# Optimization experiments

Measured on AMD Instinct MI355X. Metric: run time of the kernel, lower is better.

The kernel has to match this reference:

```python
import jax, jax.numpy as jnp
import numpy as np
from jax import lax

B, CIN, COUT, H, W = 4, 256, 256, 64, 64
KH = KW = 3
K = KH * KW
GN_GROUPS = 32
EPS = 1e-5


def setup_inputs() -> dict:
    key = jax.random.key(0)
    ks = jax.random.split(key, 6)
    x = jax.random.normal(ks[0], (B, CIN, H, W), jnp.float32)
    # offset predictor conv: 3x3, 18 out channels, with bias (init small so offsets stay near 0)
    offset_w = jax.random.normal(ks[1], (2 * K, CIN, KH, KW), jnp.float32) * 0.01
    offset_b = jax.random.normal(ks[2], (2 * K,), jnp.float32) * 0.01
    # deformable conv weight (no bias), He-ish scale
    deform_w = jax.random.normal(ks[3], (COUT, CIN, KH, KW), jnp.float32) * (1.0 / np.sqrt(CIN * K))
    gn_gamma = jnp.ones((COUT,), jnp.float32)
    gn_beta = jnp.zeros((COUT,), jnp.float32)
    return {"x": x, "offset_w": offset_w, "offset_b": offset_b,
            "deform_w": deform_w, "gn_gamma": gn_gamma, "gn_beta": gn_beta}


def _deform_conv(x, offset, weight):
    """Deformable conv v1, stride=1, pad=1, dil=1, deformable_groups=1.
    x: [B,C,H,W]; offset: [B,2K,H,W] with (dy,dx) per kernel tap; weight: [O,C,3,3].
    """
    b, c, h, w = x.shape
    off = offset.reshape(b, K, 2, h, w)
    # base sampling grid per kernel tap: p = p0 - pad + k
    ky, kx = jnp.meshgrid(jnp.arange(KH), jnp.arange(KW), indexing="ij")
    base_y = (jnp.arange(h, dtype=jnp.float32) - 1.0)[None, :, None] + ky.reshape(K).astype(jnp.float32)[:, None, None]  # [K,H,1]
    base_x = (jnp.arange(w, dtype=jnp.float32) - 1.0)[None, None, :] + kx.reshape(K).astype(jnp.float32)[:, None, None]  # [K,1,W]
    py = base_y[None] + off[:, :, 0]  # [B,K,H,W]
    px = base_x[None] + off[:, :, 1]  # [B,K,H,W]

    y0 = jnp.floor(py)
    x0 = jnp.floor(px)
    ty = py - y0
    tx = px - x0
    y0 = y0.astype(jnp.int32)
    x0 = x0.astype(jnp.int32)

    x_hw = x.transpose(0, 2, 3, 1).reshape(b, h * w, c)  # [B,HW,C]

    def corner(yi, xi, wgt):
        valid = (yi >= 0) & (yi < h) & (xi >= 0) & (xi < w)
        yc = jnp.clip(yi, 0, h - 1)
        xc = jnp.clip(xi, 0, w - 1)
        idx = (yc * w + xc).reshape(b, K * h * w)
        v = jnp.take_along_axis(x_hw, idx[..., None], axis=1)  # [B,KHW,C]
        return v * (wgt * valid.astype(wgt.dtype)).reshape(b, K * h * w, 1)

    samp = (corner(y0, x0, (1 - ty) * (1 - tx))
            + corner(y0, x0 + 1, (1 - ty) * tx)
            + corner(y0 + 1, x0, ty * (1 - tx))
            + corner(y0 + 1, x0 + 1, ty * tx))  # [B,KHW,C]
    samp = samp.reshape(b, K, h, w, c)
    return jnp.einsum("bkhwc,ock->bohw", samp, weight.reshape(weight.shape[0], c, K))


def reference(x, offset_w, offset_b, deform_w, gn_gamma, gn_beta):
    # offset = conv3x3(x) + bias
    offset = lax.conv_general_dilated(
        x, offset_w, window_strides=(1, 1), padding=((1, 1), (1, 1)),
        dimension_numbers=("NCHW", "OIHW", "NCHW")) + offset_b[None, :, None, None]
    out = _deform_conv(x, offset, deform_w)
    # GroupNorm(32, COUT) + ReLU
    b, c, h, w = out.shape
    g = out.reshape(b, GN_GROUPS, (c // GN_GROUPS) * h * w)
    mu = g.mean(axis=2, keepdims=True)
    var = g.var(axis=2, keepdims=True)
    g = (g - mu) * lax.rsqrt(var + EPS)
    out = g.reshape(b, c, h, w) * gn_gamma[None, :, None, None] + gn_beta[None, :, None, None]
    return jax.nn.relu(out)
```

## Files before the change

kernel.cpp:

```cpp
#include <hip/hip_runtime.h>
#include <hip/hip_bf16.h>
#include <stdint.h>


typedef unsigned short u16;
typedef __bf16 bf16x8 __attribute__((ext_vector_type(8)));
typedef float f32x4_t __attribute__((ext_vector_type(4)));

#define HW 4096

__device__ __forceinline__ uint32_t f32_to_bf16_rne(float f) {
  uint32_t u = __builtin_bit_cast(uint32_t, f);
  return (u + 0x7FFFu + ((u >> 16) & 1u)) >> 16;
}
__device__ __forceinline__ float bf_lo(uint32_t u) {
  return __builtin_bit_cast(float, u << 16);
}
__device__ __forceinline__ float bf_hi(uint32_t u) {
  return __builtin_bit_cast(float, u & 0xFFFF0000u);
}
__device__ __forceinline__ uint32_t blend2(uint32_t a, uint32_t b, uint32_t c,
                                           uint32_t d, float4 mw) {
  float lo = mw.x * bf_lo(a) + mw.y * bf_lo(b) + mw.z * bf_lo(c) + mw.w * bf_lo(d);
  float hi = mw.x * bf_hi(a) + mw.y * bf_hi(b) + mw.z * bf_hi(c) + mw.w * bf_hi(d);
  return f32_to_bf16_rne(lo) | (f32_to_bf16_rne(hi) << 16);
}

__global__ __launch_bounds__(256) void k_transpose(const float* __restrict__ x,
                                                   u16* __restrict__ xt) {
  __shared__ float tile[32][33];
  int b = blockIdx.z;
  int c0 = blockIdx.y * 32;
  int p0 = blockIdx.x * 32;
  int tx = threadIdx.x, ty = threadIdx.y;
#pragma unroll
  for (int j = 0; j < 32; j += 8)
    tile[ty + j][tx] = x[(b * 256 + c0 + ty + j) * HW + p0 + tx];
  __syncthreads();
  int wid = ty * 32 + tx;
  int cp = wid & 15;
  int pr = wid >> 4;
#pragma unroll
  for (int j = 0; j < 2; j++) {
    int p = pr + j * 16;
    uint32_t lo = f32_to_bf16_rne(tile[cp * 2][p]);
    uint32_t hi = f32_to_bf16_rne(tile[cp * 2 + 1][p]);
    *(uint32_t*)&xt[(b * HW + p0 + p) * 256 + c0 + cp * 2] = lo | (hi << 16);
  }
}

__global__ __launch_bounds__(256) void k_prep(const float* __restrict__ wsrc,
                                              const float* __restrict__ ow,
                                              u16* __restrict__ warr,
                                              u16* __restrict__ owm,
                                              float* __restrict__ part) {
  int bid = blockIdx.x;
  if (bid < 2304) {
    int e = bid * 256 + threadIdx.x;
    int kk = e & 7, m = (e >> 3) & 255, g = (e >> 11) & 7, kc = e >> 14;
    int cin = (kc & 3) * 64 + g * 8 + kk;
    int tap = kc >> 2;
    warr[e] = (u16)f32_to_bf16_rne(wsrc[m * 2304 + cin * 9 + tap]);
  } else if (bid < 2592) {
    int e = (bid - 2304) * 256 + threadIdx.x;
    int kk = e & 7, m = (e >> 3) & 31, g = (e >> 8) & 7, kc = e >> 11;
    int cin = (kc & 3) * 64 + g * 8 + kk;
    int tap = kc >> 2;
    float v = (m < 18) ? ow[m * 2304 + cin * 9 + tap] : 0.f;
    owm[e] = (u16)f32_to_bf16_rne(v);
  } else {
    part[threadIdx.x] = 0.f;
  }
}

__global__ __launch_bounds__(512, 4) void k_conv(
    const u16* __restrict__ xt, const u16* __restrict__ warr,
    const u16* __restrict__ owm, const float* __restrict__ ob,
    float* __restrict__ out, float* __restrict__ part) {
  __shared__ char smem[54272];
  u16* stage = (u16*)smem;
  float* off_part = (float*)(smem + 33792);
  int4* ci_s = (int4*)smem;
  float4* mw_s = (float4*)(smem + 4608);
  u16* b_s = (u16*)(smem + 9216);

  int tid = threadIdx.x;
  int lane = tid & 63;
  int wm = tid >> 6;
  int b = blockIdx.x >> 7;
  int pt = blockIdx.x & 127;
  int p0 = pt * 32;
  int yrow = p0 >> 6, xbase = p0 & 63;

  {
    u16* st = stage + wm * 2112;
    int q = lane & 15, pq = lane >> 4;
    int oct = lane & 7, pxs = lane >> 3;
    f32x4_t a2[2][2] = {};
#pragma unroll 1
    for (int kc = wm; kc < 36; kc += 8) {
      int tap = kc >> 2, cc = kc & 3;
      int ky = tap / 3, kx = tap % 3;
      int yy = yrow + ky - 1;
      bool vy = (yy >= 0) && (yy < 64);
#pragma unroll
      for (int i = 0; i < 4; i++) {
        int px = i * 8 + pxs;
        int xx2 = xbase + px + kx - 1;
        uint4 v = make_uint4(0u, 0u, 0u, 0u);
        if (vy && xx2 >= 0 && xx2 < 64)
          v = *(const uint4*)&xt[(b * HW + yy * 64 + xx2) * 256 + cc * 64 + oct * 8];
        *(uint4*)&st[oct * 264 + px * 8] = v;
      }
#pragma unroll
      for (int ks = 0; ks < 2; ks++) {
        int g = ks * 4 + pq;
        const u16* ab = owm + kc * 2048 + g * 256;
#pragma unroll
        for (int s = 0; s < 2; s++) {
          bf16x8 bfr = *(bf16x8*)&st[g * 264 + (s * 16 + q) * 8];
#pragma unroll
          for (int im = 0; im < 2; im++) {
            bf16x8 af = *(const bf16x8*)&ab[(im * 16 + q) * 8];
            a2[s][im] = __builtin_amdgcn_mfma_f32_16x16x32_bf16(af, bfr, a2[s][im], 0, 0, 0);
          }
        }
      }
    }
#pragma unroll
    for (int s = 0; s < 2; s++)
#pragma unroll
      for (int im = 0; im < 2; im++)
#pragma unroll
        for (int r = 0; r < 4; r++) {
          int oc = im * 16 + pq * 4 + r;
          if (oc < 18) off_part[(wm * 32 + s * 16 + q) * 20 + oc] = a2[s][im][r];
        }
  }
  __syncthreads();
  for (int it = tid; it < 288; it += 512) {
    int tap = it >> 5;
    int px = it & 31;
    float dy = ob[2 * tap], dx = ob[2 * tap + 1];
#pragma unroll
    for (int wv = 0; wv < 8; wv++) {
      dy += off_part[(wv * 32 + px) * 20 + 2 * tap];
      dx += off_part[(wv * 32 + px) * 20 + 2 * tap + 1];
    }
    int ky = tap / 3, kx = tap % 3;
    int p = p0 + px;
    int yq = p >> 6, xq = p & 63;
    float py = (float)(yq - 1 + ky) + dy;
    float pxx = (float)(xq - 1 + kx) + dx;
    float y0f = floorf(py), x0f = floorf(pxx);
    float ty = py - y0f, tx = pxx - x0f;
    int y0 = (int)y0f, x0 = (int)x0f;
    int y1 = y0 + 1, x1 = x0 + 1;
    float wy0 = 1.f - ty, wy1 = ty, wx0 = 1.f - tx, wx1 = tx;
    bool vy0 = (y0 >= 0) && (y0 < 64), vy1 = (y1 >= 0) && (y1 < 64);
    bool vx0 = (x0 >= 0) && (x0 < 64), vx1 = (x1 >= 0) && (x1 < 64);
    int cy0 = min(max(y0, 0), 63), cy1 = min(max(y1, 0), 63);
    int cx0 = min(max(x0, 0), 63), cx1 = min(max(x1, 0), 63);
    int base = b * HW;
    int4 ci;
    ci.x = (base + cy0 * 64 + cx0) * 256;
    ci.y = (base + cy0 * 64 + cx1) * 256;
    ci.z = (base + cy1 * 64 + cx0) * 256;
    ci.w = (base + cy1 * 64 + cx1) * 256;
    float4 mw;
    mw.x = wy0 * wx0 * ((vy0 && vx0) ? 1.f : 0.f);
    mw.y = wy0 * wx1 * ((vy0 && vx1) ? 1.f : 0.f);
    mw.z = wy1 * wx0 * ((vy1 && vx0) ? 1.f : 0.f);
    mw.w = wy1 * wx1 * ((vy1 && vx1) ? 1.f : 0.f);
    ci_s[it] = ci;
    mw_s[it] = mw;
  }
  __syncthreads();

  {
    int oct8 = tid & 15;
    int pxg = tid >> 4;
    int sub = pxg >> 4;
    int pxw = pxg & 15;
    int col = lane & 15;
    int pq = lane >> 4;
    f32x4_t acc[2][2] = {};

    int4 ci = ci_s[pxg];
    float4 mw = mw_s[pxg];
    int e = oct8 * 8;
    uint4 c0 = *(const uint4*)&xt[ci.x + e];
    uint4 c1 = *(const uint4*)&xt[ci.y + e];
    uint4 c2 = *(const uint4*)&xt[ci.z + e];
    uint4 c3 = *(const uint4*)&xt[ci.w + e];

#pragma unroll 1
    for (int dccg = 0; dccg < 18; dccg++) {
      u16* bb = b_s + (dccg & 1) * 4352;
      uint4 u;
      u.x = blend2(c0.x, c1.x, c2.x, c3.x, mw);
      u.y = blend2(c0.y, c1.y, c2.y, c3.y, mw);
      u.z = blend2(c0.z, c1.z, c2.z, c3.z, mw);
      u.w = blend2(c0.w, c1.w, c2.w, c3.w, mw);
      *(uint4*)&bb[sub * 2176 + oct8 * 136 + pxw * 8] = u;
      __syncthreads();
      if (dccg < 17) {
        int nx = dccg + 1;
        int tapn = nx >> 1;
        int en = (nx & 1) * 128 + oct8 * 8;
        int4 cin = ci_s[tapn * 32 + pxg];
        float4 mwn = mw_s[tapn * 32 + pxg];
        c0 = *(const uint4*)&xt[cin.x + en];
        c1 = *(const uint4*)&xt[cin.y + en];
        c2 = *(const uint4*)&xt[cin.z + en];
        c3 = *(const uint4*)&xt[cin.w + en];
        mw = mwn;
      }
      int tap = dccg >> 1, dcc = dccg & 1;
#pragma unroll
      for (int ks = 0; ks < 4; ks++) {
        int ro = ks * 4 + pq;
        bf16x8 b0 = *(bf16x8*)&bb[ro * 136 + col * 8];
        bf16x8 b1 = *(bf16x8*)&bb[2176 + ro * 136 + col * 8];
        int kc = tap * 4 + dcc * 2 + (ks >> 1);
        int g = (ks & 1) * 4 + pq;
        const u16* ab = warr + kc * 16384 + g * 2048 + (wm * 32 + col) * 8;
#pragma unroll
        for (int im = 0; im < 2; im++) {
          bf16x8 af = *(const bf16x8*)&ab[im * 128];
          acc[0][im] = __builtin_amdgcn_mfma_f32_16x16x32_bf16(af, b0, acc[0][im], 0, 0, 0);
          acc[1][im] = __builtin_amdgcn_mfma_f32_16x16x32_bf16(af, b1, acc[1][im], 0, 0, 0);
        }
      }
    }

#pragma unroll
    for (int im = 0; im < 2; im++) {
      float s = 0.f, ss = 0.f;
#pragma unroll
      for (int sb = 0; sb < 2; sb++) {
        int n = p0 + sb * 16 + col;
#pragma unroll
        for (int r = 0; r < 4; r++) {
          int m = wm * 32 + im * 16 + pq * 4 + r;
          float v = acc[sb][im][r];
          out[(b * 256 + m) * HW + n] = v;
          s += v;
          ss += v * v;
        }
      }
#pragma unroll
      for (int msk = 1; msk <= 16; msk <<= 1) {
        s += __shfl_xor(s, msk);
        ss += __shfl_xor(ss, msk);
      }
      if ((lane & 31) == 0) {
        int g = wm * 4 + im * 2 + (lane >> 5);
        float* pp = part + (b * 32 + g) * 2;
        atomicAdd(pp, s);
        atomicAdd(pp + 1, ss);
      }
    }
  }
}

__global__ __launch_bounds__(256) void k_gn_apply(float* __restrict__ out,
                                                  const float2* __restrict__ part,
                                                  const float* __restrict__ gamma,
                                                  const float* __restrict__ beta) {
  __shared__ float sga, sbe;
  int gid = blockIdx.x * 256 + threadIdx.x;
  int c = (gid >> 10) & 255;
  int bb = gid >> 18;
  if (threadIdx.x == 0) {
    float2 p = part[bb * 32 + (c >> 3)];
    float mu = p.x / 32768.f;
    float var = p.y / 32768.f - mu * mu;
    float rs = rsqrtf(var + 1e-5f);
    float ga = gamma[c] * rs;
    sga = ga;
    sbe = beta[c] - mu * ga;
  }
  __syncthreads();
  float ga = sga, be = sbe;
  float4 v = ((const float4*)out)[gid];
  v.x = fmaxf(v.x * ga + be, 0.f);
  v.y = fmaxf(v.y * ga + be, 0.f);
  v.z = fmaxf(v.z * ga + be, 0.f);
  v.w = fmaxf(v.w * ga + be, 0.f);
  ((float4*)out)[gid] = v;
}

extern "C" void kernel_launch(void* const* d_in, const int* in_sizes, int n_in,
                              void* d_out, int out_size, void* d_ws, size_t ws_size,
                              hipStream_t stream) {
  const float* x = (const float*)d_in[0];
  const float* offset_w = (const float*)d_in[1];
  const float* offset_b = (const float*)d_in[2];
  const float* deform_w = (const float*)d_in[3];
  const float* gn_gamma = (const float*)d_in[4];
  const float* gn_beta = (const float*)d_in[5];
  float* out = (float*)d_out;
  char* ws = (char*)d_ws;

  u16* xt = (u16*)ws;
  u16* warr = (u16*)(ws + 8388608);
  u16* owm = (u16*)(ws + 9568256);
  float* part = (float*)(ws + 9715712);

  k_transpose<<<dim3(128, 8, 4), dim3(32, 8), 0, stream>>>(x, xt);
  k_prep<<<dim3(2593), dim3(256), 0, stream>>>(deform_w, offset_w, warr, owm, part);
  k_conv<<<dim3(512), dim3(512), 0, stream>>>(xt, warr, owm, offset_b, out, part);
  k_gn_apply<<<dim3(4096), dim3(256), 0, stream>>>(out, (const float2*)part, gn_gamma, gn_beta);
}
```

Measured before the change: 163.4 us.

## Merge prep kernels, swizzle conv blocks, prefetch both halves, set MFMA priority

The transpose and weight-prep kernels are merged into one launch, removing a kernel boundary. The conv block index is remapped so neighbouring blocks land on different XCDs, and the gather loop is restructured per tap to prefetch both channel halves ahead of the GEMM. s_setprio is raised around the MFMA sections. GroupNorm apply now computes scale and shift per thread instead of going through shared memory and a barrier. These are several unrelated tweaks, and the extra prefetch registers may lower occupancy.

```diff
diff --git a/kernel.cpp b/kernel.cpp
--- a/kernel.cpp
+++ b/kernel.cpp
@@ -26,50 +26,48 @@
   return f32_to_bf16_rne(lo) | (f32_to_bf16_rne(hi) << 16);
 }
 
-__global__ __launch_bounds__(256) void k_transpose(const float* __restrict__ x,
-                                                   u16* __restrict__ xt) {
+__global__ __launch_bounds__(256) void k_pre(const float* __restrict__ x,
+                                             const float* __restrict__ wsrc,
+                                             const float* __restrict__ ow,
+                                             u16* __restrict__ xt,
+                                             u16* __restrict__ warr,
+                                             u16* __restrict__ owm,
+                                             float* __restrict__ part) {
   __shared__ float tile[32][33];
-  int b = blockIdx.z;
-  int c0 = blockIdx.y * 32;
-  int p0 = blockIdx.x * 32;
-  int tx = threadIdx.x, ty = threadIdx.y;
-#pragma unroll
-  for (int j = 0; j < 32; j += 8)
-    tile[ty + j][tx] = x[(b * 256 + c0 + ty + j) * HW + p0 + tx];
-  __syncthreads();
-  int wid = ty * 32 + tx;
-  int cp = wid & 15;
-  int pr = wid >> 4;
-#pragma unroll
-  for (int j = 0; j < 2; j++) {
-    int p = pr + j * 16;
-    uint32_t lo = f32_to_bf16_rne(tile[cp * 2][p]);
-    uint32_t hi = f32_to_bf16_rne(tile[cp * 2 + 1][p]);
-    *(uint32_t*)&xt[(b * HW + p0 + p) * 256 + c0 + cp * 2] = lo | (hi << 16);
-  }
-}
-
-__global__ __launch_bounds__(256) void k_prep(const float* __restrict__ wsrc,
-                                              const float* __restrict__ ow,
-                                              u16* __restrict__ warr,
-                                              u16* __restrict__ owm,
-                                              float* __restrict__ part) {
   int bid = blockIdx.x;
-  if (bid < 2304) {
-    int e = bid * 256 + threadIdx.x;
+  int tid = threadIdx.x;
+  if (bid < 4096) {
+    int bx = bid & 127, by = (bid >> 7) & 7, bz = bid >> 10;
+    int c0 = by * 32, p0 = bx * 32;
+    int tx = tid & 31, ty = tid >> 5;
+#pragma unroll
+    for (int j = 0; j < 32; j += 8)
+      tile[ty + j][tx] = x[(bz * 256 + c0 + ty + j) * HW + p0 + tx];
+    __syncthreads();
+    int cp = tid & 15;
+    int pr = tid >> 4;
+#pragma unroll
+    for (int j = 0; j < 2; j++) {
+      int p = pr + j * 16;
+      uint32_t lo = f32_to_bf16_rne(tile[cp * 2][p]);
+      uint32_t hi = f32_to_bf16_rne(tile[cp * 2 + 1][p]);
+      *(uint32_t*)&xt[(bz * HW + p0 + p) * 256 + c0 + cp * 2] = lo | (hi << 16);
+    }
+  } else if (bid < 6400) {
+    int e = (bid - 4096) * 256 + tid;
     int kk = e & 7, m = (e >> 3) & 255, g = (e >> 11) & 7, kc = e >> 14;
     int cin = (kc & 3) * 64 + g * 8 + kk;
     int tap = kc >> 2;
     warr[e] = (u16)f32_to_bf16_rne(wsrc[m * 2304 + cin * 9 + tap]);
-  } else if (bid < 2592) {
-    int e = (bid - 2304) * 256 + threadIdx.x;
+  } else if (bid < 6688) {
+    int e = (bid - 6400) * 256 + tid;
     int kk = e & 7, m = (e >> 3) & 31, g = (e >> 8) & 7, kc = e >> 11;
     int cin = (kc & 3) * 64 + g * 8 + kk;
     int tap = kc >> 2;
     float v = (m < 18) ? ow[m * 2304 + cin * 9 + tap] : 0.f;
     owm[e] = (u16)f32_to_bf16_rne(v);
   } else {
-    part[threadIdx.x] = 0.f;
+    part[tid] = 0.f;
   }
 }
 
@@ -87,8 +85,9 @@
   int tid = threadIdx.x;
   int lane = tid & 63;
   int wm = tid >> 6;
-  int b = blockIdx.x >> 7;
-  int pt = blockIdx.x & 127;
+  int wk = (blockIdx.x & 7) * 64 + (blockIdx.x >> 3);
+  int b = wk >> 7;
+  int pt = wk & 127;
   int p0 = pt * 32;
   int yrow = p0 >> 6, xbase = p0 & 63;
 
@@ -184,54 +183,73 @@
     int pxw = pxg & 15;
     int col = lane & 15;
     int pq = lane >> 4;
+    int e0 = oct8 * 8;
     f32x4_t acc[2][2] = {};
 
-    int4 ci = ci_s[pxg];
-    float4 mw = mw_s[pxg];
-    int e = oct8 * 8;
-    uint4 c0 = *(const uint4*)&xt[ci.x + e];
-    uint4 c1 = *(const uint4*)&xt[ci.y + e];
-    uint4 c2 = *(const uint4*)&xt[ci.z + e];
-    uint4 c3 = *(const uint4*)&xt[ci.w + e];
-
-#pragma unroll 1
-    for (int dccg = 0; dccg < 18; dccg++) {
-      u16* bb = b_s + (dccg & 1) * 4352;
+    auto stage_b = [&](uint4 c0, uint4 c1, uint4 c2, uint4 c3, float4 mw, u16* bb) {
       uint4 u;
       u.x = blend2(c0.x, c1.x, c2.x, c3.x, mw);
       u.y = blend2(c0.y, c1.y, c2.y, c3.y, mw);
       u.z = blend2(c0.z, c1.z, c2.z, c3.z, mw);
       u.w = blend2(c0.w, c1.w, c2.w, c3.w, mw);
       *(uint4*)&bb[sub * 2176 + oct8 * 136 + pxw * 8] = u;
-      __syncthreads();
-      if (dccg < 17) {
-        int nx = dccg + 1;
-        int tapn = nx >> 1;
-        int en = (nx & 1) * 128 + oct8 * 8;
-        int4 cin = ci_s[tapn * 32 + pxg];
-        float4 mwn = mw_s[tapn * 32 + pxg];
-        c0 = *(const uint4*)&xt[cin.x + en];
-        c1 = *(const uint4*)&xt[cin.y + en];
-        c2 = *(const uint4*)&xt[cin.z + en];
-        c3 = *(const uint4*)&xt[cin.w + en];
-        mw = mwn;
-      }
-      int tap = dccg >> 1, dcc = dccg & 1;
+    };
+    auto gemm = [&](const u16* bb, int kcbase) {
+      __builtin_amdgcn_s_setprio(1);
 #pragma unroll
       for (int ks = 0; ks < 4; ks++) {
         int ro = ks * 4 + pq;
-        bf16x8 b0 = *(bf16x8*)&bb[ro * 136 + col * 8];
-        bf16x8 b1 = *(bf16x8*)&bb[2176 + ro * 136 + col * 8];
-        int kc = tap * 4 + dcc * 2 + (ks >> 1);
-        int g = (ks & 1) * 4 + pq;
-        const u16* ab = warr + kc * 16384 + g * 2048 + (wm * 32 + col) * 8;
+        bf16x8 bb0 = *(bf16x8*)&bb[ro * 136 + col * 8];
+        bf16x8 bb1 = *(bf16x8*)&bb[2176 + ro * 136 + col * 8];
+        int kc = kcbase + (ks >> 1);
+        int gg = (ks & 1) * 4 + pq;
+        const u16* ab = warr + kc * 16384 + gg * 2048 + (wm * 32 + col) * 8;
 #pragma unroll
         for (int im = 0; im < 2; im++) {
           bf16x8 af = *(const bf16x8*)&ab[im * 128];
-          acc[0][im] = __builtin_amdgcn_mfma_f32_16x16x32_bf16(af, b0, acc[0][im], 0, 0, 0);
-          acc[1][im] = __builtin_amdgcn_mfma_f32_16x16x32_bf16(af, b1, acc[1][im], 0, 0, 0);
+          acc[0][im] = __builtin_amdgcn_mfma_f32_16x16x32_bf16(af, bb0, acc[0][im], 0, 0, 0);
+          acc[1][im] = __builtin_amdgcn_mfma_f32_16x16x32_bf16(af, bb1, acc[1][im], 0, 0, 0);
         }
       }
+      __builtin_amdgcn_s_setprio(0);
+    };
+
+    int4 ci0 = ci_s[pxg];
+    float4 mw_cur = mw_s[pxg];
+    uint4 a0 = *(const uint4*)&xt[ci0.x + e0];
+    uint4 a1 = *(const uint4*)&xt[ci0.y + e0];
+    uint4 a2v = *(const uint4*)&xt[ci0.z + e0];
+    uint4 a3 = *(const uint4*)&xt[ci0.w + e0];
+    uint4 g0 = *(const uint4*)&xt[ci0.x + 128 + e0];
+    uint4 g1 = *(const uint4*)&xt[ci0.y + 128 + e0];
+    uint4 g2 = *(const uint4*)&xt[ci0.z + 128 + e0];
+    uint4 g3 = *(const uint4*)&xt[ci0.w + 128 + e0];
+    float4 mw_nxt = mw_cur;
+    int4 ci_n = ci0;
+
+#pragma unroll 1
+    for (int dp = 0; dp < 9; dp++) {
+      stage_b(a0, a1, a2v, a3, mw_cur, b_s);
+      __syncthreads();
+      if (dp < 8) {
+        ci_n = ci_s[(dp + 1) * 32 + pxg];
+        mw_nxt = mw_s[(dp + 1) * 32 + pxg];
+        a0 = *(const uint4*)&xt[ci_n.x + e0];
+        a1 = *(const uint4*)&xt[ci_n.y + e0];
+        a2v = *(const uint4*)&xt[ci_n.z + e0];
+        a3 = *(const uint4*)&xt[ci_n.w + e0];
+      }
+      gemm(b_s, dp * 4);
+      stage_b(g0, g1, g2, g3, mw_cur, b_s + 4352);
+      __syncthreads();
+      if (dp < 8) {
+        g0 = *(const uint4*)&xt[ci_n.x + 128 + e0];
+        g1 = *(const uint4*)&xt[ci_n.y + 128 + e0];
+        g2 = *(const uint4*)&xt[ci_n.z + 128 + e0];
+        g3 = *(const uint4*)&xt[ci_n.w + 128 + e0];
+      }
+      gemm(b_s + 4352, dp * 4 + 2);
+      mw_cur = mw_nxt;
     }
 
 #pragma unroll
@@ -255,8 +273,8 @@
         ss += __shfl_xor(ss, msk);
       }
       if ((lane & 31) == 0) {
-        int g = wm * 4 + im * 2 + (lane >> 5);
-        float* pp = part + (b * 32 + g) * 2;
+        int grp = wm * 4 + im * 2 + (lane >> 5);
+        float* pp = part + (b * 32 + grp) * 2;
         atomicAdd(pp, s);
         atomicAdd(pp + 1, ss);
       }
@@ -268,21 +286,15 @@
                                                   const float2* __restrict__ part,
                                                   const float* __restrict__ gamma,
                                                   const float* __restrict__ beta) {
-  __shared__ float sga, sbe;
   int gid = blockIdx.x * 256 + threadIdx.x;
   int c = (gid >> 10) & 255;
   int bb = gid >> 18;
-  if (threadIdx.x == 0) {
-    float2 p = part[bb * 32 + (c >> 3)];
-    float mu = p.x / 32768.f;
-    float var = p.y / 32768.f - mu * mu;
-    float rs = rsqrtf(var + 1e-5f);
-    float ga = gamma[c] * rs;
-    sga = ga;
-    sbe = beta[c] - mu * ga;
-  }
-  __syncthreads();
-  float ga = sga, be = sbe;
+  float2 p = part[bb * 32 + (c >> 3)];
+  float mu = p.x / 32768.f;
+  float var = p.y / 32768.f - mu * mu;
+  float rs = rsqrtf(var + 1e-5f);
+  float ga = gamma[c] * rs;
+  float be = beta[c] - mu * ga;
   float4 v = ((const float4*)out)[gid];
   v.x = fmaxf(v.x * ga + be, 0.f);
   v.y = fmaxf(v.y * ga + be, 0.f);
@@ -308,8 +320,7 @@
   u16* owm = (u16*)(ws + 9568256);
   float* part = (float*)(ws + 9715712);
 
-  k_transpose<<<dim3(128, 8, 4), dim3(32, 8), 0, stream>>>(x, xt);
-  k_prep<<<dim3(2593), dim3(256), 0, stream>>>(deform_w, offset_w, warr, owm, part);
+  k_pre<<<dim3(6689), dim3(256), 0, stream>>>(x, deform_w, offset_w, xt, warr, owm, part);
   k_conv<<<dim3(512), dim3(512), 0, stream>>>(xt, warr, owm, offset_b, out, part);
   k_gn_apply<<<dim3(4096), dim3(256), 0, stream>>>(out, (const float2*)part, gn_gamma, gn_beta);
 }
```

New measurement: 157.7 us. 3.5% less time.
